# Performance work log

Hardware: AMD Instinct MI355X
Metric: run time of the kernel (lower is better)

## Reference

```python
import jax, jax.numpy as jnp
import numpy as np

K_NBR = 128        # PyG radius(max_num_neighbors=128)
NEG_FILL = -1e9    # mask value for max-aggregation over invalid neighbors


def fps(pos, m):
    # Farthest point sampling on pos [N,2] -> [m] int32 indices (start at 0).
    n = pos.shape[0]
    def step(carry, _):
        min_d2, last = carry
        d2 = jnp.sum((pos - pos[last]) ** 2, axis=-1)
        min_d2 = jnp.minimum(min_d2, d2)
        nxt = jnp.argmax(min_d2).astype(jnp.int32)
        return (min_d2, nxt), nxt
    init = (jnp.full((n,), 1e10, pos.dtype), jnp.int32(0))
    _, idxs = jax.lax.scan(step, init, None, length=m - 1)
    return jnp.concatenate([jnp.zeros((1,), jnp.int32), idxs])


def set_abstraction(x, pos, ratio, r, W, b):
    # x [B,N,C], pos [B,N,2]. FPS centers, radius neighbors (<=K), PointNetConv
    # message = Linear(cat[x_j, pos_j - pos_i]) (PyG MLP with one layer and
    # plain_last=True is a bare Linear), then max-aggregate per center.
    B, N, C = x.shape
    m = int(N * ratio)
    idx = jax.vmap(lambda p: fps(p, m))(pos)                         # [B,m]
    ctr = jnp.take_along_axis(pos, idx[..., None], axis=1)           # [B,m,2]
    d2 = jnp.sum((ctr[:, :, None, :] - pos[:, None, :, :]) ** 2, -1)  # [B,m,N]
    k = min(K_NBR, N)
    neg_d2, nbr = jax.lax.top_k(-d2, k)                              # [B,m,k]
    valid = (-neg_d2) <= r * r                                       # in-radius mask
    gather = jax.vmap(lambda a, i: a[i])                             # per-sample fancy index
    x_j = gather(x, nbr)                                             # [B,m,k,C]
    rel = gather(pos, nbr) - ctr[:, :, None, :]                      # [B,m,k,2]
    msg = jnp.concatenate([x_j, rel], axis=-1) @ W + b               # [B,m,k,F]
    msg = jnp.where(valid[..., None], msg, NEG_FILL)
    return jnp.max(msg, axis=2), ctr                                 # [B,m,F], [B,m,2]


def encoder(x, zones_ids, lf_W1, lf_b1, lf_W2, lf_b2, c1_W, c1_b, c2_W, c2_b, c3_W, c3_b):
    lf = jnp.tanh(jnp.tanh(x @ lf_W1 + lf_b1) @ lf_W2 + lf_b2)       # [B,N,64]
    h = jnp.concatenate([lf, zones_ids], axis=-1)                    # [B,N,65]
    h, pos = set_abstraction(h, x, 0.5, 0.5, c1_W, c1_b)             # [B,N/2,64]
    h, pos = set_abstraction(h, pos, 0.25, 1.0, c2_W, c2_b)          # [B,N/8,128]
    g = jnp.concatenate([h, pos], axis=-1) @ c3_W + c3_b             # [B,N/8,1024]
    gf = jnp.max(g, axis=1, keepdims=True)                           # global max pool -> [B,1,1024]
    return lf, gf


def setup_inputs():
    key = jax.random.key(0)
    ks = jax.random.split(key, 12)
    B, N = 4, 4096
    def lin(kw, kb, fi, fo):
        return (jax.random.normal(kw, (fi, fo), jnp.float32) / np.sqrt(fi),
                jax.random.normal(kb, (fo,), jnp.float32) * 0.01)
    x = jax.random.normal(ks[0], (B, N, 2), jnp.float32) * 4.0  # spread so ball(r) holds <128 pts
    zones_ids = jax.random.uniform(ks[1], (B, N, 1), jnp.float32)
    lf_W1, lf_b1 = lin(ks[2], ks[3], 2, 64)
    lf_W2, lf_b2 = lin(ks[4], ks[5], 64, 64)
    c1_W, c1_b = lin(ks[6], ks[7], 67, 64)
    c2_W, c2_b = lin(ks[8], ks[9], 66, 128)
    c3_W, c3_b = lin(ks[10], ks[11], 130, 1024)
    return {"x": x, "zones_ids": zones_ids, "lf_W1": lf_W1, "lf_b1": lf_b1,
            "lf_W2": lf_W2, "lf_b2": lf_b2, "c1_W": c1_W, "c1_b": c1_b,
            "c2_W": c2_W, "c2_b": c2_b, "c3_W": c3_W, "c3_b": c3_b}


def reference(x, zones_ids, lf_W1, lf_b1, lf_W2, lf_b2, c1_W, c1_b, c2_W, c2_b, c3_W, c3_b):
    return encoder(x, zones_ids, lf_W1, lf_b1, lf_W2, lf_b2,
                   c1_W, c1_b, c2_W, c2_b, c3_W, c3_b)
```

## Files before the change

### kernel.cpp

```cpp
#include <hip/hip_runtime.h>


constexpr int BB = 4;
constexpr int NN = 4096;
constexpr int M1 = 2048;
constexpr int M2 = 512;

typedef float v2f __attribute__((ext_vector_type(2)));

__device__ __forceinline__ float d2_exact(float dx, float dy) {
    return __fadd_rn(__fmul_rn(dx, dx), __fmul_rn(dy, dy));
}

template<int CTRL>
__device__ __forceinline__ unsigned long long dpp64z(unsigned long long v) {
    unsigned lo = (unsigned)__builtin_amdgcn_update_dpp(0, (int)(unsigned)v, CTRL, 0xF, 0xF, true);
    unsigned hi = (unsigned)__builtin_amdgcn_update_dpp(0, (int)(unsigned)(v >> 32), CTRL, 0xF, 0xF, true);
    return ((unsigned long long)hi << 32) | (unsigned long long)lo;
}
template<int CTRL>
__device__ __forceinline__ void pairc(unsigned long long& t1, unsigned long long& t2) {
    unsigned long long o1 = dpp64z<CTRL>(t1);
    unsigned long long o2 = dpp64z<CTRL>(t2);
    bool g = o1 > t1;
    unsigned long long m1 = g ? o1 : t1;
    unsigned long long sm = g ? t1 : o1;
    unsigned long long cn = g ? o2 : t2;
    t2 = cn > sm ? cn : sm;
    t1 = m1;
}

template<int M, int PPT>
__device__ __forceinline__ void fps_core(
    const float2* __restrict__ src, const float2* __restrict__ PTSl,
    float2* __restrict__ centl, uint4 (&slk)[2][4],
    int tid, int lane, int wv)
{
#pragma clang fp contract(off)
    constexpr int PP2 = PPT / 2;
    v2f px2[PP2], py2[PP2], md2[PP2];
#pragma unroll
    for (int k = 0; k < PP2; ++k) {
        float2 a = src[tid + (2 * k) * 256];
        float2 b = src[tid + (2 * k + 1) * 256];
        px2[k] = (v2f){a.x, b.x};
        py2[k] = (v2f){a.y, b.y};
        md2[k] = (v2f){1e10f, 1e10f};
    }
    float2 c0 = src[0];
    if (tid == 0) centl[0] = c0;

    unsigned baseu = 0xFFFFFFFFu - (unsigned)tid;
    float c1x = c0.x, c1y = c0.y, c2x = 0.0f, c2y = 0.0f;
    bool two = false;
    int it = 1;
    unsigned rc = 0;
    while (it < M) {
        int par = (int)(rc & 1u); ++rc;
        v2f vcx = (v2f){c1x, c1x}, vcy = (v2f){c1y, c1y};
#pragma unroll
        for (int k = 0; k < PP2; ++k) {
            v2f dx = px2[k] - vcx, dy = py2[k] - vcy;
            v2f d2 = (dx * dx) + (dy * dy);
            md2[k] = __builtin_elementwise_min(md2[k], d2);
        }
        if (two) {
            v2f wcx = (v2f){c2x, c2x}, wcy = (v2f){c2y, c2y};
#pragma unroll
            for (int k = 0; k < PP2; ++k) {
                v2f dx = px2[k] - wcx, dy = py2[k] - wcy;
                v2f d2 = (dx * dx) + (dy * dy);
                md2[k] = __builtin_elementwise_min(md2[k], d2);
            }
        }
        float t1f = -1.0f, t2f = -1.0f;
        unsigned i1 = 0u, i2 = 0u;
#pragma unroll
        for (int s = 0; s < PPT; ++s) {
            float mq = (s & 1) ? md2[s >> 1].y : md2[s >> 1].x;
            unsigned io = baseu - (unsigned)(s * 256);
            bool g1 = mq > t1f;
            bool g2 = mq > t2f;
            t2f = g1 ? t1f : (g2 ? mq : t2f);
            i2  = g1 ? i1  : (g2 ? io : i2);
            t1f = g1 ? mq : t1f;
            i1  = g1 ? io : i1;
        }
        unsigned long long t1 =
            ((unsigned long long)__float_as_uint(t1f) << 32) | (unsigned long long)i1;
        unsigned long long t2 =
            ((unsigned long long)__float_as_uint(t2f) << 32) | (unsigned long long)i2;
        pairc<0x111>(t1, t2); pairc<0x112>(t1, t2); pairc<0x114>(t1, t2);
        pairc<0x118>(t1, t2); pairc<0x142>(t1, t2); pairc<0x143>(t1, t2);
        if (lane == 63)
            slk[par][wv] = make_uint4((unsigned)t1, (unsigned)(t1 >> 32),
                                      (unsigned)t2, (unsigned)(t2 >> 32));
        __syncthreads();
        uint4 e = slk[par][lane & 3];
        unsigned long long a1 = ((unsigned long long)e.y << 32) | (unsigned long long)e.x;
        unsigned long long a2 = ((unsigned long long)e.w << 32) | (unsigned long long)e.z;
        pairc<0xB1>(a1, a2);
        pairc<0x4E>(a1, a2);
        int jw = (int)(0xFFFFFFFFu - (unsigned)a1);
        int jr = (int)(0xFFFFFFFFu - (unsigned)a2);
        float mdr = __uint_as_float((unsigned)(a2 >> 32));
        float2 wpt = PTSl[jw];
        float2 rpt = PTSl[jr];
        float ddx = rpt.x - wpt.x, ddy = rpt.y - wpt.y;
        float dd = (ddx * ddx) + (ddy * ddy);
        bool dbl = (it + 1 < M) && (dd >= mdr);
        if (tid == 0) { centl[it] = wpt; if (dbl) centl[it + 1] = rpt; }
        c1x = wpt.x; c1y = wpt.y; c2x = rpt.x; c2y = rpt.y;
        two = dbl;
        it += dbl ? 2 : 1;
    }
}

__global__ __launch_bounds__(256, 1) void k_fps1(
    const float2* __restrict__ pos, float* __restrict__ p1out,
    const float* __restrict__ zones,
    const float* __restrict__ W1, const float* __restrict__ b1,
    const float* __restrict__ W2, const float* __restrict__ b2,
    const float* __restrict__ c1W, const float* __restrict__ c1b,
    float* __restrict__ out_lf, float* __restrict__ y1)
{
    __shared__ float2 PTS[NN];
    __shared__ float2 cent1[M1];
    __shared__ uint4 slk[2][4];
    __shared__ float2 LPAD[4160];
    int tid = threadIdx.x, lane = tid & 63, wv = tid >> 6;
    if (blockIdx.x == 0xFFFFFFFFu) { LPAD[0] = PTS[0]; p1out[0] = LPAD[0].x; }

    if (blockIdx.x >= (unsigned)BB) {
        float* sh = (float*)PTS;
        float* sl = sh + 256;
        int p = tid >> 6, f = tid & 63;
        size_t pt = (size_t)(blockIdx.x - BB) * 4 + p;
        float2 xv = pos[pt];
        float hid = tanhf(xv.x * W1[f] + xv.y * W1[64 + f] + b1[f]);
        sh[p * 64 + f] = hid;
        __syncthreads();
        float acc = b2[f];
#pragma unroll
        for (int c = 0; c < 64; ++c) acc += sh[p * 64 + c] * W2[c * 64 + f];
        float lf = tanhf(acc);
        sl[p * 64 + f] = lf;
        out_lf[pt * 64 + f] = lf;
        __syncthreads();
        float acc2 = c1b[f] + zones[pt] * c1W[64 * 64 + f]
                   + xv.x * c1W[65 * 64 + f] + xv.y * c1W[66 * 64 + f];
#pragma unroll
        for (int c = 0; c < 64; ++c) acc2 += sl[p * 64 + c] * c1W[c * 64 + f];
        y1[pt * 64 + f] = acc2;
        return;
    }

    const float2* p = pos + (size_t)blockIdx.x * NN;
    for (int i = tid; i < NN; i += 256) PTS[i] = p[i];
    __syncthreads();

    fps_core<M1, NN / 256>(p, PTS, cent1, slk, tid, lane, wv);
    __syncthreads();
    float2* o1 = (float2*)(p1out + (size_t)blockIdx.x * M1 * 2);
    for (int i = tid; i < M1; i += 256) o1[i] = cent1[i];
}

__global__ __launch_bounds__(256) void k_fps2_sa1(
    const float2* __restrict__ x, const float* __restrict__ p1,
    const float* __restrict__ y1, const float* __restrict__ c1W,
    const float* __restrict__ c2W, const float* __restrict__ c2b,
    float* __restrict__ p2out, float* __restrict__ h1,
    float* __restrict__ y2, int fuse_y2)
{
    __shared__ float2 PTS2[M1];
    __shared__ float2 cent2[M2];
    __shared__ uint4 slk[2][4];
    __shared__ int cnt;
    __shared__ int list[NN];
    __shared__ float h1row[64];
    int tid = threadIdx.x, lane = tid & 63, wv = tid >> 6;

    if (blockIdx.x < (unsigned)BB) {
        const float2* p1b = (const float2*)(p1 + (size_t)blockIdx.x * M1 * 2);
        for (int i = tid; i < M1; i += 256) PTS2[i] = p1b[i];
        __syncthreads();
        fps_core<M2, M1 / 256>(PTS2, PTS2, cent2, slk, tid, lane, wv);
        __syncthreads();
        float2* o2 = (float2*)(p2out + (size_t)blockIdx.x * M2 * 2);
        for (int i = tid; i < M2; i += 256) o2[i] = cent2[i];
        return;
    }

    int idx = (int)blockIdx.x - BB;
    int b = idx >> 11;
    size_t crow = (size_t)idx;
    if (tid == 0) cnt = 0;
    __syncthreads();
    float cx = p1[crow * 2], cy = p1[crow * 2 + 1];
    const float2* cp = x + (size_t)b * NN;
    for (int j = tid; j < NN; j += 256) {
        float2 pj = cp[j];
        float d2 = d2_exact(pj.x - cx, pj.y - cy);
        if (d2 <= 0.25f) { int t = atomicAdd(&cnt, 1); list[t] = j; }
    }
    __syncthreads();
    int n = cnt;
    for (int f = tid; f < 64; f += 256) {
        float m = -3.0e38f;
        for (int t = 0; t < n; ++t)
            m = fmaxf(m, y1[((size_t)b * NN + list[t]) * 64 + f]);
        float ct = cx * c1W[(size_t)65 * 64 + f] + cy * c1W[(size_t)66 * 64 + f];
        float h1v = m - ct;
        if (fuse_y2) h1row[f] = h1v;
        else h1[crow * 64 + f] = h1v;
    }
    if (fuse_y2) {
        __syncthreads();
        for (int f = tid; f < 128; f += 256) {
            float acc = c2b[f] + cx * c2W[64 * 128 + f]
                      + cy * c2W[65 * 128 + f];
#pragma unroll
            for (int c = 0; c < 64; ++c) acc += h1row[c] * c2W[c * 128 + f];
            y2[crow * 128 + f] = acc;
        }
    }
}

__global__ __launch_bounds__(256) void k_sa(
    const float2* __restrict__ candpos, const float* __restrict__ y,
    const float* __restrict__ ctr, const float* __restrict__ W,
    int NP, int F, int relrow, float r2, float* __restrict__ hout)
{
    __shared__ int cnt;
    __shared__ int list[4096];
    int tid = threadIdx.x;
    int b = blockIdx.y;
    size_t crow = (size_t)b * gridDim.x + blockIdx.x;
    if (tid == 0) cnt = 0;
    __syncthreads();
    float cx = ctr[crow * 2], cy = ctr[crow * 2 + 1];
    const float2* cp = candpos + (size_t)b * NP;
    for (int j = tid; j < NP; j += 256) {
        float2 pj = cp[j];
        float d2 = d2_exact(pj.x - cx, pj.y - cy);
        if (d2 <= r2) { int t = atomicAdd(&cnt, 1); list[t] = j; }
    }
    __syncthreads();
    int n = cnt;
    for (int f = tid; f < F; f += 256) {
        float m = -3.0e38f;
        for (int t = 0; t < n; ++t)
            m = fmaxf(m, y[((size_t)b * NP + list[t]) * F + f]);
        float ct = cx * W[(size_t)relrow * F + f] + cy * W[(size_t)(relrow + 1) * F + f];
        hout[crow * F + f] = m - ct;
    }
}

__global__ __launch_bounds__(128) void k_y2(
    const float* __restrict__ h1, const float* __restrict__ p1,
    const float* __restrict__ W, const float* __restrict__ bb,
    float* __restrict__ y2)
{
    __shared__ float sh[64];
    size_t row = blockIdx.x;
    int f = threadIdx.x;
    if (f < 64) sh[f] = h1[row * 64 + f];
    __syncthreads();
    float acc = bb[f] + p1[row * 2] * W[64 * 128 + f]
              + p1[row * 2 + 1] * W[65 * 128 + f];
#pragma unroll
    for (int c = 0; c < 64; ++c) acc += sh[c] * W[c * 128 + f];
    y2[row * 128 + f] = acc;
}

__global__ __launch_bounds__(256) void k_g(
    const float* __restrict__ h2, const float* __restrict__ p2,
    const float* __restrict__ W3, const float* __restrict__ b3,
    float* __restrict__ part)
{
    int f = blockIdx.x * 256 + threadIdx.x;
    int b = blockIdx.z;
    int i0 = blockIdx.y * 8;
    float acc[8];
    float bbv = b3[f];
#pragma unroll
    for (int ii = 0; ii < 8; ++ii) acc[ii] = bbv;
    const float* hrow = h2 + ((size_t)b * M2 + i0) * 128;
    for (int c = 0; c < 128; ++c) {
        float w = W3[(size_t)c * 1024 + f];
#pragma unroll
        for (int ii = 0; ii < 8; ++ii) acc[ii] += hrow[ii * 128 + c] * w;
    }
    float wx = W3[(size_t)128 * 1024 + f];
    float wy = W3[(size_t)129 * 1024 + f];
    const float* prow = p2 + ((size_t)b * M2 + i0) * 2;
    float m = -3.0e38f;
#pragma unroll
    for (int ii = 0; ii < 8; ++ii) {
        float g = acc[ii] + prow[ii * 2] * wx + prow[ii * 2 + 1] * wy;
        m = fmaxf(m, g);
    }
    part[((size_t)b * 64 + blockIdx.y) * 1024 + f] = m;
}

__global__ __launch_bounds__(256) void k_gmax(const float* __restrict__ part,
                                              float* __restrict__ outg)
{
    int f = blockIdx.x * 256 + threadIdx.x;
    int b = f >> 10, fl = f & 1023;
    float m = -3.0e38f;
#pragma unroll 8
    for (int ig = 0; ig < 64; ++ig)
        m = fmaxf(m, part[((size_t)b * 64 + ig) * 1024 + fl]);
    outg[f] = m;
}

extern "C" void kernel_launch(void* const* d_in, const int* in_sizes, int n_in,
                              void* d_out, int out_size, void* d_ws, size_t ws_size,
                              hipStream_t stream)
{
    const float* x    = (const float*)d_in[0];
    const float* zon  = (const float*)d_in[1];
    const float* lfW1 = (const float*)d_in[2];
    const float* lfb1 = (const float*)d_in[3];
    const float* lfW2 = (const float*)d_in[4];
    const float* lfb2 = (const float*)d_in[5];
    const float* c1W  = (const float*)d_in[6];
    const float* c1b  = (const float*)d_in[7];
    const float* c2W  = (const float*)d_in[8];
    const float* c2b  = (const float*)d_in[9];
    const float* c3W  = (const float*)d_in[10];
    const float* c3b  = (const float*)d_in[11];
    float* out = (float*)d_out;

    const size_t szY1 = (size_t)BB * NN * 64 * 4;
    const size_t szP1 = (size_t)BB * M1 * 2 * 4;
    const size_t szH1 = (size_t)BB * M1 * 64 * 4;
    const size_t szY2 = (size_t)BB * M1 * 128 * 4;
    const size_t szP2 = (size_t)BB * M2 * 2 * 4;
    const size_t szH2 = (size_t)BB * M2 * 128 * 4;

    bool fuse = ws_size >= szY1 + szP1 + szY2 + szP2 + szH2;

    char* w = (char*)d_ws;
    float* y1 = (float*)w;                     w += szY1;
    float* p1 = (float*)w;                     w += szP1;
    float *h1, *y2;
    if (fuse) {
        h1 = nullptr;
        y2 = (float*)w;                        w += szY2;
    } else {
        h1 = (float*)w;                        w += szH1;
        y2 = y1;
    }
    float* p2 = (float*)w;                     w += szP2;
    float* h2 = (float*)w;                     w += szH2;
    float* part = y1;

    k_fps1<<<BB + BB * NN / 4, 256, 0, stream>>>(
        (const float2*)x, p1, zon, lfW1, lfb1, lfW2, lfb2, c1W, c1b, out, y1);
    k_fps2_sa1<<<BB + BB * M1, 256, 0, stream>>>(
        (const float2*)x, p1, y1, c1W, c2W, c2b, p2,
        fuse ? p1  : h1, y2, fuse ? 1 : 0);
    if (!fuse)
        k_y2<<<BB * M1, 128, 0, stream>>>(h1, p1, c2W, c2b, y2);
    k_sa<<<dim3(M2, BB), 256, 0, stream>>>((const float2*)p1, y2, p2, c2W,
                                           M1, 128, 64, 1.0f, h2);
    k_g<<<dim3(4, 64, BB), 256, 0, stream>>>(h2, p2, c3W, c3b, part);
    k_gmax<<<16, 256, 0, stream>>>(part, out + (size_t)BB * NN * 64);
}
```

Measured before the change: 1.429 ms.

## Extend FPS speculative selection from top-2 to top-3 candidates per round

```diff
diff --git a/kernel.cpp b/kernel.cpp
--- a/kernel.cpp
+++ b/kernel.cpp
@@ -19,21 +19,29 @@
     return ((unsigned long long)hi << 32) | (unsigned long long)lo;
 }
 template<int CTRL>
-__device__ __forceinline__ void pairc(unsigned long long& t1, unsigned long long& t2) {
-    unsigned long long o1 = dpp64z<CTRL>(t1);
-    unsigned long long o2 = dpp64z<CTRL>(t2);
-    bool g = o1 > t1;
-    unsigned long long m1 = g ? o1 : t1;
-    unsigned long long sm = g ? t1 : o1;
-    unsigned long long cn = g ? o2 : t2;
-    t2 = cn > sm ? cn : sm;
-    t1 = m1;
+__device__ __forceinline__ void tric(unsigned long long& t1,
+                                     unsigned long long& t2,
+                                     unsigned long long& t3) {
+    unsigned long long b1 = dpp64z<CTRL>(t1);
+    unsigned long long b2 = dpp64z<CTRL>(t2);
+    unsigned long long b3 = dpp64z<CTRL>(t3);
+    bool g = b1 > t1;
+    unsigned long long m1 = g ? b1 : t1;
+    unsigned long long s1 = g ? t1 : b1;
+    unsigned long long w2 = g ? b2 : t2;
+    unsigned long long w3 = g ? b3 : t3;
+    unsigned long long l2 = g ? t2 : b2;
+    bool h = w2 > s1;
+    unsigned long long m2 = h ? w2 : s1;
+    unsigned long long m3 = h ? (w3 > s1 ? w3 : s1)
+                             : (w2 > l2 ? w2 : l2);
+    t1 = m1; t2 = m2; t3 = m3;
 }
 
 template<int M, int PPT>
 __device__ __forceinline__ void fps_core(
     const float2* __restrict__ src, const float2* __restrict__ PTSl,
-    float2* __restrict__ centl, uint4 (&slk)[2][4],
+    float2* __restrict__ centl, uint4 (&slkA)[2][4], uint2 (&slkB)[2][4],
     int tid, int lane, int wv)
 {
 #pragma clang fp contract(off)
@@ -51,8 +59,9 @@
     if (tid == 0) centl[0] = c0;
 
     unsigned baseu = 0xFFFFFFFFu - (unsigned)tid;
-    float c1x = c0.x, c1y = c0.y, c2x = 0.0f, c2y = 0.0f;
-    bool two = false;
+    float c1x = c0.x, c1y = c0.y;
+    float c2x = 0.0f, c2y = 0.0f, c3x = 0.0f, c3y = 0.0f;
+    bool two = false, three = false;
     int it = 1;
     unsigned rc = 0;
     while (it < M) {
@@ -73,14 +82,26 @@
                 md2[k] = __builtin_elementwise_min(md2[k], d2);
             }
         }
-        float t1f = -1.0f, t2f = -1.0f;
-        unsigned i1 = 0u, i2 = 0u;
+        if (three) {
+            v2f tcx = (v2f){c3x, c3x}, tcy = (v2f){c3y, c3y};
+#pragma unroll
+            for (int k = 0; k < PP2; ++k) {
+                v2f dx = px2[k] - tcx, dy = py2[k] - tcy;
+                v2f d2 = (dx * dx) + (dy * dy);
+                md2[k] = __builtin_elementwise_min(md2[k], d2);
+            }
+        }
+        float t1f = -1.0f, t2f = -1.0f, t3f = -1.0f;
+        unsigned i1 = 0u, i2 = 0u, i3 = 0u;
 #pragma unroll
         for (int s = 0; s < PPT; ++s) {
             float mq = (s & 1) ? md2[s >> 1].y : md2[s >> 1].x;
             unsigned io = baseu - (unsigned)(s * 256);
             bool g1 = mq > t1f;
             bool g2 = mq > t2f;
+            bool g3 = mq > t3f;
+            t3f = g2 ? t2f : (g3 ? mq : t3f);
+            i3  = g2 ? i2  : (g3 ? io : i3);
             t2f = g1 ? t1f : (g2 ? mq : t2f);
             i2  = g1 ? i1  : (g2 ? io : i2);
             t1f = g1 ? mq : t1f;
@@ -90,29 +111,51 @@
             ((unsigned long long)__float_as_uint(t1f) << 32) | (unsigned long long)i1;
         unsigned long long t2 =
             ((unsigned long long)__float_as_uint(t2f) << 32) | (unsigned long long)i2;
-        pairc<0x111>(t1, t2); pairc<0x112>(t1, t2); pairc<0x114>(t1, t2);
-        pairc<0x118>(t1, t2); pairc<0x142>(t1, t2); pairc<0x143>(t1, t2);
-        if (lane == 63)
-            slk[par][wv] = make_uint4((unsigned)t1, (unsigned)(t1 >> 32),
-                                      (unsigned)t2, (unsigned)(t2 >> 32));
-        __syncthreads();
-        uint4 e = slk[par][lane & 3];
-        unsigned long long a1 = ((unsigned long long)e.y << 32) | (unsigned long long)e.x;
-        unsigned long long a2 = ((unsigned long long)e.w << 32) | (unsigned long long)e.z;
-        pairc<0xB1>(a1, a2);
-        pairc<0x4E>(a1, a2);
+        unsigned long long t3 =
+            ((unsigned long long)__float_as_uint(t3f) << 32) | (unsigned long long)i3;
+        tric<0x111>(t1, t2, t3); tric<0x112>(t1, t2, t3);
+        tric<0x114>(t1, t2, t3); tric<0x118>(t1, t2, t3);
+        tric<0x142>(t1, t2, t3); tric<0x143>(t1, t2, t3);
+        if (lane == 63) {
+            slkA[par][wv] = make_uint4((unsigned)t1, (unsigned)(t1 >> 32),
+                                       (unsigned)t2, (unsigned)(t2 >> 32));
+            slkB[par][wv] = make_uint2((unsigned)t3, (unsigned)(t3 >> 32));
+        }
+        __syncthreads();
+        uint4 eA = slkA[par][lane & 3];
+        uint2 eB = slkB[par][lane & 3];
+        unsigned long long a1 = ((unsigned long long)eA.y << 32) | (unsigned long long)eA.x;
+        unsigned long long a2 = ((unsigned long long)eA.w << 32) | (unsigned long long)eA.z;
+        unsigned long long a3 = ((unsigned long long)eB.y << 32) | (unsigned long long)eB.x;
+        tric<0xB1>(a1, a2, a3);
+        tric<0x4E>(a1, a2, a3);
         int jw = (int)(0xFFFFFFFFu - (unsigned)a1);
         int jr = (int)(0xFFFFFFFFu - (unsigned)a2);
+        int jt = (int)(0xFFFFFFFFu - (unsigned)a3);
         float mdr = __uint_as_float((unsigned)(a2 >> 32));
+        float mdt = __uint_as_float((unsigned)(a3 >> 32));
         float2 wpt = PTSl[jw];
         float2 rpt = PTSl[jr];
+        float2 tpt = PTSl[jt];
         float ddx = rpt.x - wpt.x, ddy = rpt.y - wpt.y;
         float dd = (ddx * ddx) + (ddy * ddy);
-        bool dbl = (it + 1 < M) && (dd >= mdr);
-        if (tid == 0) { centl[it] = wpt; if (dbl) centl[it + 1] = rpt; }
-        c1x = wpt.x; c1y = wpt.y; c2x = rpt.x; c2y = rpt.y;
+        float twx = tpt.x - wpt.x, twy = tpt.y - wpt.y;
+        float dtw = (twx * twx) + (twy * twy);
+        float trx = tpt.x - rpt.x, try_ = tpt.y - rpt.y;
+        float dtr = (trx * trx) + (try_ * try_);
+        bool dbl  = (it + 1 < M) && (dd >= mdr);
+        bool trip = dbl && (it + 2 < M) && (dtw >= mdt) && (dtr >= mdt);
+        if (tid == 0) {
+            centl[it] = wpt;
+            if (dbl)  centl[it + 1] = rpt;
+            if (trip) centl[it + 2] = tpt;
+        }
+        c1x = wpt.x; c1y = wpt.y;
+        c2x = rpt.x; c2y = rpt.y;
+        c3x = tpt.x; c3y = tpt.y;
         two = dbl;
-        it += dbl ? 2 : 1;
+        three = trip;
+        it += trip ? 3 : (dbl ? 2 : 1);
     }
 }
 
@@ -126,10 +169,9 @@
 {
     __shared__ float2 PTS[NN];
     __shared__ float2 cent1[M1];
-    __shared__ uint4 slk[2][4];
-    __shared__ float2 LPAD[4160];
+    __shared__ uint4 slkA[2][4];
+    __shared__ uint2 slkB[2][4];
     int tid = threadIdx.x, lane = tid & 63, wv = tid >> 6;
-    if (blockIdx.x == 0xFFFFFFFFu) { LPAD[0] = PTS[0]; p1out[0] = LPAD[0].x; }
 
     if (blockIdx.x >= (unsigned)BB) {
         float* sh = (float*)PTS;
@@ -159,7 +201,7 @@
     for (int i = tid; i < NN; i += 256) PTS[i] = p[i];
     __syncthreads();
 
-    fps_core<M1, NN / 256>(p, PTS, cent1, slk, tid, lane, wv);
+    fps_core<M1, NN / 256>(p, PTS, cent1, slkA, slkB, tid, lane, wv);
     __syncthreads();
     float2* o1 = (float2*)(p1out + (size_t)blockIdx.x * M1 * 2);
     for (int i = tid; i < M1; i += 256) o1[i] = cent1[i];
@@ -174,7 +216,8 @@
 {
     __shared__ float2 PTS2[M1];
     __shared__ float2 cent2[M2];
-    __shared__ uint4 slk[2][4];
+    __shared__ uint4 slkA[2][4];
+    __shared__ uint2 slkB[2][4];
     __shared__ int cnt;
     __shared__ int list[NN];
     __shared__ float h1row[64];
@@ -184,7 +227,7 @@
         const float2* p1b = (const float2*)(p1 + (size_t)blockIdx.x * M1 * 2);
         for (int i = tid; i < M1; i += 256) PTS2[i] = p1b[i];
         __syncthreads();
-        fps_core<M2, M1 / 256>(PTS2, PTS2, cent2, slk, tid, lane, wv);
+        fps_core<M2, M1 / 256>(PTS2, PTS2, cent2, slkA, slkB, tid, lane, wv);
         __syncthreads();
         float2* o2 = (float2*)(p2out + (size_t)blockIdx.x * M2 * 2);
         for (int i = tid; i < M2; i += 256) o2[i] = cent2[i];
```

Measured after the change: 1.443 ms. About the same (+1.0%).
